# Kernel tuning notes

Measured on AMD Instinct MI355X. Metric: run time of the kernel, lower is better.

## Reference

```python
import jax, jax.numpy as jnp
import numpy as np

N = 50000      # nodes per type
E = 800000     # edges per relation
D = 128        # input feature dim
H = 128        # hidden_channels


def setup_inputs() -> dict:
    key = jax.random.key(0)
    ks = jax.random.split(key, 20)
    f = lambda k, shp: jax.random.normal(k, shp, dtype=jnp.float32) * 0.05
    inp = {
        "x_ligand": jax.random.normal(ks[0], (N, D), dtype=jnp.float32),
        "x_protein": jax.random.normal(ks[1], (N, D), dtype=jnp.float32),
        "ei_lp": jax.random.randint(ks[2], (2, E), 0, N, dtype=jnp.int64),
        "ei_pp": jax.random.randint(ks[3], (2, E), 0, N, dtype=jnp.int64),
        "ei_ll": jax.random.randint(ks[4], (2, E), 0, N, dtype=jnp.int64),
        "Wl_lp": f(ks[5], (D, H)), "bl_lp": f(ks[6], (H,)), "Wr_lp": f(ks[7], (D, H)),
        "Wl_pp": f(ks[8], (D, H)), "bl_pp": f(ks[9], (H,)), "Wr_pp": f(ks[10], (D, H)),
        "Wl_ll": f(ks[11], (D, H)), "bl_ll": f(ks[12], (H,)), "Wr_ll": f(ks[13], (D, H)),
        "W_out": f(ks[14], (H, 1)), "b_out": f(ks[15], (1,)),
    }
    return inp


def _sage(x_src, x_dst, edge_index, Wl, bl, Wr):
    # PyG SAGEConv: mean-aggregate neighbor (src) features onto dst, then
    # out = lin_l(agg) + lin_r(x_dst)  (lin_l has bias, lin_r does not)
    src, dst = edge_index[0], edge_index[1]
    n_dst = x_dst.shape[0]
    msgs = x_src[src]                                      # [E, D] gather
    s = jax.ops.segment_sum(msgs, dst, num_segments=n_dst) # [N_dst, D]
    cnt = jax.ops.segment_sum(jnp.ones((edge_index.shape[1],), x_src.dtype),
                              dst, num_segments=n_dst)     # [N_dst]
    agg = s / jnp.maximum(cnt, 1.0)[:, None]               # mean, 0 if isolated
    return agg @ Wl + bl + x_dst @ Wr


def reference(x_ligand, x_protein, ei_lp, ei_pp, ei_ll,
              Wl_lp, bl_lp, Wr_lp, Wl_pp, bl_pp, Wr_pp,
              Wl_ll, bl_ll, Wr_ll, W_out, b_out):
    # HeteroConv: sum contributions per destination node type
    protein_out = (_sage(x_ligand, x_protein, ei_lp, Wl_lp, bl_lp, Wr_lp)
                   + _sage(x_protein, x_protein, ei_pp, Wl_pp, bl_pp, Wr_pp))
    ligand_out = _sage(x_ligand, x_ligand, ei_ll, Wl_ll, bl_ll, Wr_ll)
    # relu per node type; only ligand is used downstream
    lig = jax.nn.relu(ligand_out).mean(axis=0)             # [H]
    _ = jax.nn.relu(protein_out)                           # computed in original
    return lig @ W_out + b_out                             # [1]
```

## Files before the change

### kernel.cpp

```cpp
#include <hip/hip_runtime.h>
#include <hip/hip_bf16.h>

#define DIM 128
#define EPB 4096
#define NRBIN 1024
#define RCAP 1280

typedef __attribute__((ext_vector_type(8))) short bf16x8;
typedef __attribute__((ext_vector_type(4))) float f32x4;
typedef __attribute__((ext_vector_type(4))) short short4v;
typedef __attribute__((ext_vector_type(4))) int int4v;

__device__ inline unsigned short f2bf(float f) {
  union { float f; unsigned u; } v; v.f = f;
  return (unsigned short)((v.u + 0x7FFFu + ((v.u >> 16) & 1u)) >> 16);
}
__device__ inline float lo_f(unsigned u) {
  union { unsigned u; float f; } v; v.u = u << 16; return v.f;
}
__device__ inline float hi_f(unsigned u) {
  union { unsigned u; float f; } v; v.u = u & 0xFFFF0000u; return v.f;
}

__global__ __launch_bounds__(256) void prep_part_kernel(
    const int* __restrict__ ei, unsigned* __restrict__ chunkbuf,
    int* __restrict__ startsT, int* __restrict__ countsT, int E, int nchunk,
    const float* __restrict__ x, short* __restrict__ A,
    const float* __restrict__ Wl, const float* __restrict__ Wr,
    short* __restrict__ Bpack, int nnodes, int mpad, int xb) {
  __shared__ unsigned uns[EPB];
  __shared__ unsigned srt[EPB];
  __shared__ int lhist[NRBIN];
  __shared__ int lstart[NRBIN];
  __shared__ int tsum[256];
  const int tid = threadIdx.x;
  const int bid = blockIdx.x;

  if (bid >= nchunk) {
    if (bid < nchunk + xb) {
      int t = (bid - nchunk) * 256 + tid;
      int node = t >> 5;
      if (node >= mpad) return;
      int c = (t & 31) * 4;
      short4v o = (short4v){0, 0, 0, 0};
      if (node < nnodes) {
        float4 v = *reinterpret_cast<const float4*>(x + (size_t)node * DIM + c);
        o.x = (short)f2bf(v.x); o.y = (short)f2bf(v.y);
        o.z = (short)f2bf(v.z); o.w = (short)f2bf(v.w);
      }
      *reinterpret_cast<short4v*>(A + (size_t)node * 256 + 128 + c) = o;
    } else {
      int t = (bid - nchunk - xb) * 256 + tid;
      if (t >= 4096) return;
      int lane = t & 63, nt = (t >> 6) & 7, ks = t >> 9;
      int c = nt * 16 + (lane & 15);
      int kb = ks * 32 + ((lane >> 4) << 3);
      bf16x8 o;
#pragma unroll
      for (int j = 0; j < 8; ++j) {
        int k = kb + j;
        float v = (k < DIM) ? Wl[k * DIM + c] : Wr[(k - DIM) * DIM + c];
        o[j] = (short)f2bf(v);
      }
      reinterpret_cast<bf16x8*>(Bpack)[(ks * 8 + nt) * 64 + lane] = o;
    }
    return;
  }

  const int chunk = bid;
  const int base = chunk * EPB;
  const int count = min(EPB, E - base);

#pragma unroll
  for (int r = 0; r < NRBIN / 256; ++r) lhist[tid + 256 * r] = 0;
  __syncthreads();

  for (int r = 0; r < EPB / 1024; ++r) {
    int i = r * 1024 + tid * 4;
    if (i + 3 < count) {
      int4 s4 = *reinterpret_cast<const int4*>(ei + base + i);
      int4 d4 = *reinterpret_cast<const int4*>(ei + E + base + i);
      int ss[4] = {s4.x, s4.y, s4.z, s4.w};
      int dd[4] = {d4.x, d4.y, d4.z, d4.w};
#pragma unroll
      for (int k = 0; k < 4; ++k) {
        unsigned reg = (unsigned)dd[k] >> 6;
        uns[i + k] = (reg << 22) | ((unsigned)(dd[k] & 63) << 16) | (unsigned)ss[k];
        atomicAdd(&lhist[reg], 1);
      }
    } else {
      for (int k = 0; k < 4; ++k) {
        if (i + k < count) {
          int s = ei[base + i + k], d = ei[E + base + i + k];
          unsigned reg = (unsigned)d >> 6;
          uns[i + k] = (reg << 22) | ((unsigned)(d & 63) << 16) | (unsigned)s;
          atomicAdd(&lhist[reg], 1);
        }
      }
    }
  }
  __syncthreads();

  int h0 = lhist[tid * 4], h1 = lhist[tid * 4 + 1];
  int h2 = lhist[tid * 4 + 2], h3 = lhist[tid * 4 + 3];
  int local = h0 + h1 + h2 + h3;
  tsum[tid] = local;
  __syncthreads();
  for (int o = 1; o < 256; o <<= 1) {
    int t = (tid >= o) ? tsum[tid - o] : 0;
    __syncthreads();
    tsum[tid] += t;
    __syncthreads();
  }
  int tb = tsum[tid] - local;
  lstart[tid * 4]     = tb;
  lstart[tid * 4 + 1] = tb + h0;
  lstart[tid * 4 + 2] = tb + h0 + h1;
  lstart[tid * 4 + 3] = tb + h0 + h1 + h2;
  lhist[tid * 4] = 0; lhist[tid * 4 + 1] = 0;
  lhist[tid * 4 + 2] = 0; lhist[tid * 4 + 3] = 0;
  __syncthreads();

  for (int i = tid; i < count; i += 256) {
    unsigned e = uns[i];
    unsigned reg = e >> 22;
    int pos = lstart[reg] + atomicAdd(&lhist[reg], 1);
    srt[pos] = e;
  }
  __syncthreads();

  for (int r = 0; r < EPB / 1024; ++r) {
    int i = r * 1024 + tid * 4;
    if (i + 3 < count) {
      int4v v = {(int)srt[i], (int)srt[i + 1], (int)srt[i + 2], (int)srt[i + 3]};
      *reinterpret_cast<int4v*>(chunkbuf + (size_t)chunk * EPB + i) = v;
    } else {
      for (int k = 0; k < 4; ++k)
        if (i + k < count) chunkbuf[(size_t)chunk * EPB + i + k] = srt[i + k];
    }
  }
  for (int r = tid; r < NRBIN; r += 256) {
    startsT[(size_t)chunk * NRBIN + r] = lstart[r];
    countsT[(size_t)chunk * NRBIN + r] = lhist[r];
  }
}

__global__ __launch_bounds__(256) void compact_kernel(
    const unsigned* __restrict__ chunkbuf, const int* __restrict__ startsT,
    const int* __restrict__ countsT, int nchunk, unsigned* __restrict__ csr,
    int* __restrict__ cnt, int* __restrict__ off) {
  __shared__ unsigned raw[RCAP];
  __shared__ unsigned srt[RCAP];
  __shared__ int h[64];
  __shared__ int start[64];
  __shared__ int tsum[256];
  const int region = blockIdx.x;
  const int tid = threadIdx.x;

  int cn = 0, st = 0;
  if (tid < nchunk) {
    cn = countsT[(size_t)tid * NRBIN + region];
    st = startsT[(size_t)tid * NRBIN + region];
  }
  tsum[tid] = cn;
  __syncthreads();
  for (int o = 1; o < 256; o <<= 1) {
    int t = (tid >= o) ? tsum[tid - o] : 0;
    __syncthreads();
    tsum[tid] += t;
    __syncthreads();
  }
  const int pfx = tsum[tid] - cn;
  int total = min(tsum[255], RCAP);

  const unsigned* src = chunkbuf + (size_t)tid * EPB + st;
  for (int j = 0; j < cn && pfx + j < RCAP; ++j) raw[pfx + j] = src[j];
  if (tid < 64) h[tid] = 0;
  __syncthreads();

  for (int i = tid; i < total; i += 256) atomicAdd(&h[(raw[i] >> 16) & 63], 1);
  __syncthreads();
  if (tid == 0) {
    int s = 0;
    for (int i = 0; i < 64; ++i) { start[i] = s; s += h[i]; }
  }
  __syncthreads();
  if (tid < 64) {
    int node = region * 64 + tid;
    cnt[node] = h[tid];
    off[node] = region * RCAP + start[tid];
    h[tid] = 0;
  }
  __syncthreads();
  for (int i = tid; i < total; i += 256) {
    unsigned e = raw[i];
    int d = (e >> 16) & 63;
    int pos = start[d] + atomicAdd(&h[d], 1);
    srt[pos] = e & 0xFFFFu;
  }
  __syncthreads();
  for (int i = tid; i < total; i += 256) csr[(size_t)region * RCAP + i] = srt[i];
}

__global__ __launch_bounds__(256, 4) void agg_kernel(
    const int* __restrict__ cnt, const int* __restrict__ off,
    const unsigned* __restrict__ bucket, short* __restrict__ A,
    int nnodes, int mpad) {
  const int wid = (blockIdx.x * 256 + threadIdx.x) >> 6;
  const int lane = threadIdx.x & 63;
  if (wid >= mpad) return;
  unsigned* dst = reinterpret_cast<unsigned*>(A + (size_t)wid * 256) + lane;
  if (wid >= nnodes) { *dst = 0u; return; }
  const int deg  = __builtin_amdgcn_readfirstlane(cnt[wid]);
  const int base = __builtin_amdgcn_readfirstlane(off[wid]);
  const unsigned* xs = reinterpret_cast<const unsigned*>(A) + 64 + lane;

  unsigned ent = (lane < deg) ? bucket[base + lane] : 0u;
  const int dcap = min(deg, 64);

  float l0 = 0.f, h0 = 0.f, l1 = 0.f, h1 = 0.f;
  int j = 0;
  for (; j + 15 < dcap; j += 16) {
    unsigned u[16];
#pragma unroll
    for (int k = 0; k < 16; ++k) {
      int s = __builtin_amdgcn_readlane((int)ent, j + k);
      u[k] = xs[(size_t)s * 128];
    }
#pragma unroll
    for (int k = 0; k < 16; ++k) {
      if (k & 1) { l1 += lo_f(u[k]); h1 += hi_f(u[k]); }
      else       { l0 += lo_f(u[k]); h0 += hi_f(u[k]); }
    }
  }
  for (; j + 7 < dcap; j += 8) {
    unsigned u[8];
#pragma unroll
    for (int k = 0; k < 8; ++k) {
      int s = __builtin_amdgcn_readlane((int)ent, j + k);
      u[k] = xs[(size_t)s * 128];
    }
#pragma unroll
    for (int k = 0; k < 8; ++k) {
      if (k & 1) { l1 += lo_f(u[k]); h1 += hi_f(u[k]); }
      else       { l0 += lo_f(u[k]); h0 += hi_f(u[k]); }
    }
  }
  for (; j < dcap; ++j) {
    int s = __builtin_amdgcn_readlane((int)ent, j);
    unsigned u0 = xs[(size_t)s * 128];
    l0 += lo_f(u0); h0 += hi_f(u0);
  }
  for (; j < deg; ++j) {
    int s = __builtin_amdgcn_readfirstlane((int)bucket[base + j]);
    unsigned u0 = xs[(size_t)s * 128];
    l0 += lo_f(u0); h0 += hi_f(u0);
  }
  const float r = 1.0f / fmaxf((float)deg, 1.0f);
  const float av = (l0 + l1) * r;
  const float bv = (h0 + h1) * r;
  *dst = (unsigned)f2bf(av) | ((unsigned)f2bf(bv) << 16);
}

__global__ __launch_bounds__(256) void mfma_kernel(
    const short* __restrict__ A, const short* __restrict__ Bpack,
    const float* __restrict__ bl, float* __restrict__ partial, int nnodes) {
  __shared__ short a_lds[64 * 256];
  const int tid = threadIdx.x;
  const int wave = tid >> 6, lane = tid & 63;
  const int mt = blockIdx.x;
  const size_t abase = (size_t)mt * 64 * 256;

#pragma unroll
  for (int r = 0; r < 8; ++r) {
    int i = tid + 256 * r;
    int row = i >> 5, kc = i & 31;
    bf16x8 v = *reinterpret_cast<const bf16x8*>(A + abase + row * 256 + kc * 8);
    int byte = (row * 512 + kc * 16) ^ ((row & 7) << 4);
    *reinterpret_cast<bf16x8*>(reinterpret_cast<char*>(a_lds) + byte) = v;
  }
  __syncthreads();

  f32x4 acc[8];
#pragma unroll
  for (int nt = 0; nt < 8; ++nt) acc[nt] = (f32x4){0.f, 0.f, 0.f, 0.f};

  const int arow = wave * 16 + (lane & 15);
  const int kgrp = lane >> 4;
  const bf16x8* Bp = reinterpret_cast<const bf16x8*>(Bpack);

#pragma unroll
  for (int ks = 0; ks < 8; ++ks) {
    int byte = (arow * 512 + (ks * 32 + kgrp * 8) * 2) ^ ((arow & 7) << 4);
    bf16x8 a = *reinterpret_cast<const bf16x8*>(reinterpret_cast<char*>(a_lds) + byte);
#pragma unroll
    for (int nt = 0; nt < 8; ++nt) {
      bf16x8 b = Bp[(ks * 8 + nt) * 64 + lane];
      acc[nt] = __builtin_amdgcn_mfma_f32_16x16x32_bf16(a, b, acc[nt], 0, 0, 0);
    }
  }

  const int col16 = lane & 15;
  const int rowbase = mt * 64 + wave * 16 + kgrp * 4;
#pragma unroll
  for (int nt = 0; nt < 8; ++nt) {
    const int c = nt * 16 + col16;
    const float bb = bl[c];
    float s = 0.f;
#pragma unroll
    for (int rg = 0; rg < 4; ++rg) {
      float v = fmaxf(acc[nt][rg] + bb, 0.f);
      s += (rowbase + rg < nnodes) ? v : 0.f;
    }
    s += __shfl_xor(s, 16);
    s += __shfl_xor(s, 32);
    if (kgrp == 0) partial[((size_t)mt * 4 + wave) * DIM + c] = s;
  }
}

__global__ __launch_bounds__(256) void red1_kernel(
    const float* __restrict__ partial, int nrows, float* __restrict__ red) {
  __shared__ float tmp[128];
  const int c = threadIdx.x & 127;
  const int half = threadIdx.x >> 7;
  const int chunk = (nrows + 127) / 128;
  const int r0 = blockIdx.x * chunk;
  const int r1 = min(r0 + chunk, nrows);
  float s = 0.f;
  for (int r = r0 + half; r < r1; r += 2) s += partial[(size_t)r * DIM + c];
  if (half) tmp[c] = s;
  __syncthreads();
  if (!half) red[(size_t)blockIdx.x * DIM + c] = s + tmp[c];
}

__global__ __launch_bounds__(256) void red2_kernel(
    const float* __restrict__ red, const float* __restrict__ Wout,
    const float* __restrict__ bout, float* __restrict__ out, int nnodes) {
  __shared__ float tmp[128];
  __shared__ float prod[128];
  const int c = threadIdx.x & 127;
  const int half = threadIdx.x >> 7;
  float s = 0.f;
  for (int r = half; r < 128; r += 2) s += red[(size_t)r * DIM + c];
  if (half) tmp[c] = s;
  __syncthreads();
  if (!half) prod[c] = (s + tmp[c]) * Wout[c];
  __syncthreads();
  if (threadIdx.x == 0) {
    float v = 0.f;
    for (int i = 0; i < 128; ++i) v += prod[i];
    out[0] = v / (float)nnodes + bout[0];
  }
}

extern "C" void kernel_launch(void* const* d_in, const int* in_sizes, int n_in,
                              void* d_out, int out_size, void* d_ws, size_t ws_size,
                              hipStream_t stream) {
  const float* x    = (const float*)d_in[0];
  const int*   ei   = (const int*)d_in[4];
  const float* Wl   = (const float*)d_in[11];
  const float* bl   = (const float*)d_in[12];
  const float* Wr   = (const float*)d_in[13];
  const float* Wout = (const float*)d_in[14];
  const float* bout = (const float*)d_in[15];

  const int nnodes = in_sizes[0] / DIM;
  const int E = in_sizes[4] / 2;
  const int mtiles = (nnodes + 63) / 64;
  const int mpad = mtiles * 64;
  const int nchunk = (E + EPB - 1) / EPB;

  unsigned* chunkbuf = (unsigned*)d_ws;
  int*      startsT  = (int*)(chunkbuf + (size_t)nchunk * EPB);
  int*      countsT  = startsT + (size_t)nchunk * NRBIN;
  unsigned* csr      = (unsigned*)(countsT + (size_t)nchunk * NRBIN);
  int*      cnt      = (int*)(csr + (size_t)mtiles * RCAP);
  int*      off      = cnt + mpad;
  short*    A        = (short*)(off + mpad);
  short*    Bpack    = A + (size_t)mpad * 256;
  float*    red      = (float*)(Bpack + 32768);
  float*    partial  = (float*)chunkbuf;

  const int xb = mpad / 8;
  prep_part_kernel<<<nchunk + xb + 16, 256, 0, stream>>>(
      ei, chunkbuf, startsT, countsT, E, nchunk,
      x, A, Wl, Wr, Bpack, nnodes, mpad, xb);

  compact_kernel<<<mtiles, 256, 0, stream>>>(chunkbuf, startsT, countsT, nchunk,
                                             csr, cnt, off);

  agg_kernel<<<(mpad + 3) / 4, 256, 0, stream>>>(cnt, off, csr, A, nnodes, mpad);

  mfma_kernel<<<mtiles, 256, 0, stream>>>(A, Bpack, bl, partial, nnodes);

  red1_kernel<<<128, 256, 0, stream>>>(partial, mtiles * 4, red);
  red2_kernel<<<1, 256, 0, stream>>>(red, Wout, bout, (float*)d_out, nnodes);
}
```

Measured before the change: 91.11 us.

## Fuse neighbor aggregation into MFMA kernel, writing aggregated rows directly to LDS

```diff
diff --git a/kernel.cpp b/kernel.cpp
--- a/kernel.cpp
+++ b/kernel.cpp
@@ -48,7 +48,7 @@
         o.x = (short)f2bf(v.x); o.y = (short)f2bf(v.y);
         o.z = (short)f2bf(v.z); o.w = (short)f2bf(v.w);
       }
-      *reinterpret_cast<short4v*>(A + (size_t)node * 256 + 128 + c) = o;
+      *reinterpret_cast<short4v*>(A + (size_t)node * DIM + c) = o;
     } else {
       int t = (bid - nchunk - xb) * 256 + tid;
       if (t >= 4096) return;
@@ -202,90 +202,92 @@
   for (int i = tid; i < total; i += 256) csr[(size_t)region * RCAP + i] = srt[i];
 }
 
-__global__ __launch_bounds__(256, 4) void agg_kernel(
+__global__ __launch_bounds__(512) void aggmm_kernel(
     const int* __restrict__ cnt, const int* __restrict__ off,
-    const unsigned* __restrict__ bucket, short* __restrict__ A,
-    int nnodes, int mpad) {
-  const int wid = (blockIdx.x * 256 + threadIdx.x) >> 6;
-  const int lane = threadIdx.x & 63;
-  if (wid >= mpad) return;
-  unsigned* dst = reinterpret_cast<unsigned*>(A + (size_t)wid * 256) + lane;
-  if (wid >= nnodes) { *dst = 0u; return; }
-  const int deg  = __builtin_amdgcn_readfirstlane(cnt[wid]);
-  const int base = __builtin_amdgcn_readfirstlane(off[wid]);
-  const unsigned* xs = reinterpret_cast<const unsigned*>(A) + 64 + lane;
-
-  unsigned ent = (lane < deg) ? bucket[base + lane] : 0u;
-  const int dcap = min(deg, 64);
-
-  float l0 = 0.f, h0 = 0.f, l1 = 0.f, h1 = 0.f;
-  int j = 0;
-  for (; j + 15 < dcap; j += 16) {
-    unsigned u[16];
-#pragma unroll
-    for (int k = 0; k < 16; ++k) {
-      int s = __builtin_amdgcn_readlane((int)ent, j + k);
-      u[k] = xs[(size_t)s * 128];
-    }
-#pragma unroll
-    for (int k = 0; k < 16; ++k) {
-      if (k & 1) { l1 += lo_f(u[k]); h1 += hi_f(u[k]); }
-      else       { l0 += lo_f(u[k]); h0 += hi_f(u[k]); }
-    }
-  }
-  for (; j + 7 < dcap; j += 8) {
-    unsigned u[8];
-#pragma unroll
-    for (int k = 0; k < 8; ++k) {
-      int s = __builtin_amdgcn_readlane((int)ent, j + k);
-      u[k] = xs[(size_t)s * 128];
-    }
-#pragma unroll
-    for (int k = 0; k < 8; ++k) {
-      if (k & 1) { l1 += lo_f(u[k]); h1 += hi_f(u[k]); }
-      else       { l0 += lo_f(u[k]); h0 += hi_f(u[k]); }
-    }
-  }
-  for (; j < dcap; ++j) {
-    int s = __builtin_amdgcn_readlane((int)ent, j);
-    unsigned u0 = xs[(size_t)s * 128];
-    l0 += lo_f(u0); h0 += hi_f(u0);
-  }
-  for (; j < deg; ++j) {
-    int s = __builtin_amdgcn_readfirstlane((int)bucket[base + j]);
-    unsigned u0 = xs[(size_t)s * 128];
-    l0 += lo_f(u0); h0 += hi_f(u0);
-  }
-  const float r = 1.0f / fmaxf((float)deg, 1.0f);
-  const float av = (l0 + l1) * r;
-  const float bv = (h0 + h1) * r;
-  *dst = (unsigned)f2bf(av) | ((unsigned)f2bf(bv) << 16);
-}
-
-__global__ __launch_bounds__(256) void mfma_kernel(
-    const short* __restrict__ A, const short* __restrict__ Bpack,
-    const float* __restrict__ bl, float* __restrict__ partial, int nnodes) {
+    const unsigned* __restrict__ bucket, const short* __restrict__ A,
+    const short* __restrict__ Bpack, const float* __restrict__ bl,
+    float* __restrict__ partial, int nnodes) {
   __shared__ short a_lds[64 * 256];
   const int tid = threadIdx.x;
-  const int wave = tid >> 6, lane = tid & 63;
+  const int wave = tid >> 6;
+  const int lane = tid & 63;
   const int mt = blockIdx.x;
-  const size_t abase = (size_t)mt * 64 * 256;
-
-#pragma unroll
-  for (int r = 0; r < 8; ++r) {
-    int i = tid + 256 * r;
-    int row = i >> 5, kc = i & 31;
-    bf16x8 v = *reinterpret_cast<const bf16x8*>(A + abase + row * 256 + kc * 8);
+  const unsigned* xs = reinterpret_cast<const unsigned*>(A) + lane;
+
+  for (int n = 0; n < 8; ++n) {
+    const int row = wave * 8 + n;
+    const int node = mt * 64 + row;
+    float l0 = 0.f, h0 = 0.f, l1 = 0.f, h1 = 0.f;
+    float r = 0.f;
+    if (node < nnodes) {
+      const int deg  = __builtin_amdgcn_readfirstlane(cnt[node]);
+      const int base = __builtin_amdgcn_readfirstlane(off[node]);
+      unsigned ent = (lane < deg) ? bucket[base + lane] : 0u;
+      const int dcap = min(deg, 64);
+      int j = 0;
+      for (; j + 15 < dcap; j += 16) {
+        unsigned u[16];
+#pragma unroll
+        for (int k = 0; k < 16; ++k) {
+          int s = __builtin_amdgcn_readlane((int)ent, j + k);
+          u[k] = xs[(size_t)s * 64];
+        }
+#pragma unroll
+        for (int k = 0; k < 16; ++k) {
+          if (k & 1) { l1 += lo_f(u[k]); h1 += hi_f(u[k]); }
+          else       { l0 += lo_f(u[k]); h0 += hi_f(u[k]); }
+        }
+      }
+      for (; j + 7 < dcap; j += 8) {
+        unsigned u[8];
+#pragma unroll
+        for (int k = 0; k < 8; ++k) {
+          int s = __builtin_amdgcn_readlane((int)ent, j + k);
+          u[k] = xs[(size_t)s * 64];
+        }
+#pragma unroll
+        for (int k = 0; k < 8; ++k) {
+          if (k & 1) { l1 += lo_f(u[k]); h1 += hi_f(u[k]); }
+          else       { l0 += lo_f(u[k]); h0 += hi_f(u[k]); }
+        }
+      }
+      for (; j < dcap; ++j) {
+        int s = __builtin_amdgcn_readlane((int)ent, j);
+        unsigned u0 = xs[(size_t)s * 64];
+        l0 += lo_f(u0); h0 += hi_f(u0);
+      }
+      for (; j < deg; ++j) {
+        int s = __builtin_amdgcn_readfirstlane((int)bucket[base + j]);
+        unsigned u0 = xs[(size_t)s * 64];
+        l0 += lo_f(u0); h0 += hi_f(u0);
+      }
+      r = 1.0f / fmaxf((float)deg, 1.0f);
+    }
+    const unsigned o = (unsigned)f2bf((l0 + l1) * r) |
+                       ((unsigned)f2bf((h0 + h1) * r) << 16);
+    int byte = ((row * 512 + (lane >> 2) * 16) ^ ((row & 7) << 4)) + (lane & 3) * 4;
+    *reinterpret_cast<unsigned*>(reinterpret_cast<char*>(a_lds) + byte) = o;
+  }
+
+#pragma unroll
+  for (int rr = 0; rr < 2; ++rr) {
+    int i = tid + 512 * rr;
+    int row = i >> 4;
+    int kc = 16 + (i & 15);
+    bf16x8 v = *reinterpret_cast<const bf16x8*>(
+        A + (size_t)(mt * 64 + row) * DIM + (kc - 16) * 8);
     int byte = (row * 512 + kc * 16) ^ ((row & 7) << 4);
     *reinterpret_cast<bf16x8*>(reinterpret_cast<char*>(a_lds) + byte) = v;
   }
   __syncthreads();
 
-  f32x4 acc[8];
-#pragma unroll
-  for (int nt = 0; nt < 8; ++nt) acc[nt] = (f32x4){0.f, 0.f, 0.f, 0.f};
-
-  const int arow = wave * 16 + (lane & 15);
+  f32x4 acc[4];
+#pragma unroll
+  for (int nt = 0; nt < 4; ++nt) acc[nt] = (f32x4){0.f, 0.f, 0.f, 0.f};
+
+  const int stripe = wave >> 1;
+  const int ntbase = (wave & 1) * 4;
+  const int arow = stripe * 16 + (lane & 15);
   const int kgrp = lane >> 4;
   const bf16x8* Bp = reinterpret_cast<const bf16x8*>(Bpack);
 
@@ -294,17 +296,17 @@
     int byte = (arow * 512 + (ks * 32 + kgrp * 8) * 2) ^ ((arow & 7) << 4);
     bf16x8 a = *reinterpret_cast<const bf16x8*>(reinterpret_cast<char*>(a_lds) + byte);
 #pragma unroll
-    for (int nt = 0; nt < 8; ++nt) {
-      bf16x8 b = Bp[(ks * 8 + nt) * 64 + lane];
+    for (int nt = 0; nt < 4; ++nt) {
+      bf16x8 b = Bp[(ks * 8 + ntbase + nt) * 64 + lane];
       acc[nt] = __builtin_amdgcn_mfma_f32_16x16x32_bf16(a, b, acc[nt], 0, 0, 0);
     }
   }
 
   const int col16 = lane & 15;
-  const int rowbase = mt * 64 + wave * 16 + kgrp * 4;
-#pragma unroll
-  for (int nt = 0; nt < 8; ++nt) {
-    const int c = nt * 16 + col16;
+  const int rowbase = mt * 64 + stripe * 16 + kgrp * 4;
+#pragma unroll
+  for (int nt = 0; nt < 4; ++nt) {
+    const int c = (ntbase + nt) * 16 + col16;
     const float bb = bl[c];
     float s = 0.f;
 #pragma unroll
@@ -314,7 +316,7 @@
     }
     s += __shfl_xor(s, 16);
     s += __shfl_xor(s, 32);
-    if (kgrp == 0) partial[((size_t)mt * 4 + wave) * DIM + c] = s;
+    if (kgrp == 0) partial[((size_t)mt * 4 + stripe) * DIM + c] = s;
   }
 }
 
@@ -377,7 +379,7 @@
   int*      cnt      = (int*)(csr + (size_t)mtiles * RCAP);
   int*      off      = cnt + mpad;
   short*    A        = (short*)(off + mpad);
-  short*    Bpack    = A + (size_t)mpad * 256;
+  short*    Bpack    = A + (size_t)mpad * DIM;
   float*    red      = (float*)(Bpack + 32768);
   float*    partial  = (float*)chunkbuf;
 
@@ -389,9 +391,8 @@
   compact_kernel<<<mtiles, 256, 0, stream>>>(chunkbuf, startsT, countsT, nchunk,
                                              csr, cnt, off);
 
-  agg_kernel<<<(mpad + 3) / 4, 256, 0, stream>>>(cnt, off, csr, A, nnodes, mpad);
-
-  mfma_kernel<<<mtiles, 256, 0, stream>>>(A, Bpack, bl, partial, nnodes);
+  aggmm_kernel<<<mtiles, 512, 0, stream>>>(cnt, off, csr, A, Bpack, bl,
+                                           partial, nnodes);
 
   red1_kernel<<<128, 256, 0, stream>>>(partial, mtiles * 4, red);
   red2_kernel<<<1, 256, 0, stream>>>(red, Wout, bout, (float*)d_out, nnodes);
```

New measurement: 88.34 us. 1.03x faster.
